# Performance work log

Hardware: AMD Instinct MI355X
Metric: run time of the kernel (lower is better)

The kernel has to match this reference:

```python
import jax, jax.numpy as jnp
import numpy as np

LRELU = 0.01  # torch nn.LeakyReLU default slope

def _lrelu(x):
    return jnp.where(x >= 0, x, LRELU * x)

def setup_inputs() -> dict:
    key = jax.random.key(0)
    ks = jax.random.split(key, 10)
    B, Cin, Cout, H, W, K, FD, LAT = 16, 256, 256, 64, 64, 3, 128, 128
    y = jax.random.normal(ks[0], (B, Cin, H, W), jnp.float32)
    finger = jax.random.randint(ks[1], (B, FD), 0, 2).astype(jnp.float32)
    ori_weight = jax.random.normal(ks[2], (Cout, Cin, K, K), jnp.float32) * 0.05
    w_mask = jax.random.normal(ks[3], (Cout, Cin, 1, 1), jnp.float32)
    f_weight = ori_weight[None]  # param initialized as 1*ori_weight, shape [1,Cout,Cin,K,K]
    style_w1 = jax.random.normal(ks[4], (LAT, FD), jnp.float32) / np.sqrt(FD)
    style_w2 = jax.random.normal(ks[5], (2 * Cin * K * K, LAT), jnp.float32) / np.sqrt(LAT)
    ori_bias = jax.random.normal(ks[6], (Cout,), jnp.float32) * 0.05
    b_mask = jax.random.normal(ks[7], (Cout,), jnp.float32)
    f_bias = ori_bias[None]  # [1,Cout]
    bias_w1 = jax.random.normal(ks[8], (Cout, FD), jnp.float32) / np.sqrt(FD)
    bias_w2 = jax.random.normal(ks[9], (Cout, Cout), jnp.float32) / np.sqrt(Cout)
    return dict(y=y, finger=finger, ori_weight=ori_weight, w_mask=w_mask,
                f_weight=f_weight, style_w1=style_w1, style_w2=style_w2,
                ori_bias=ori_bias, b_mask=b_mask, f_bias=f_bias,
                bias_w1=bias_w1, bias_w2=bias_w2)

def reference(y, finger, ori_weight, w_mask, f_weight, style_w1, style_w2,
              ori_bias, b_mask, f_bias, bias_w1, bias_w2):
    B = y.shape[0]
    Cout, Cin, K, _ = ori_weight.shape
    relu6 = lambda v: jnp.clip(v, 0.0, 6.0)
    # mask blending coefficients (w_mask broadcasts over the KxK taps, as in .repeat)
    f_w_weight = (6.0 - relu6(w_mask)) / 6.0          # [Cout,Cin,1,1]
    f_w_bias = (6.0 - relu6(b_mask)) / 6.0            # [Cout]
    mean_ori = ori_weight.mean()
    std_ori = jnp.std(ori_weight, ddof=1)             # torch .std() is unbiased
    # ApplyStyle: finger -> LAT -> 2*Cin*K*K scale/shift applied to f_weight
    h = _lrelu(finger @ style_w1.T)                   # [B,LAT]
    style = (h @ style_w2.T).reshape(B, 2, 1, Cin, K, K)
    s_weight = f_weight * (style[:, 0] + 1.0) + style[:, 1]  # [B,Cout,Cin,K,K]
    fw = f_w_weight[None]
    w1 = (1.0 - fw) * ori_weight[None] + fw * s_weight
    # per-sample whole-tensor re-standardization to ori stats
    mean = w1.mean(axis=(1, 2, 3, 4), keepdims=True)
    std = jnp.std(w1, axis=(1, 2, 3, 4), keepdims=True, ddof=1)
    w2 = (w1 - mean) / std * std_ori + mean_ori
    new_weight = (1.0 - fw) * ori_weight[None] + fw * w2      # [B,Cout,Cin,K,K]
    # per-sample bias
    s_bias = f_bias * _lrelu(_lrelu(finger @ bias_w1.T) @ bias_w2.T)  # [B,Cout]
    new_bias = (1.0 - f_w_bias) * ori_bias + f_w_bias * s_bias        # [B,Cout]
    pad = K // 2
    def conv_one(xi, wi, bi):
        o = jax.lax.conv_general_dilated(xi[None], wi, (1, 1),
                                         [(pad, pad), (pad, pad)],
                                         dimension_numbers=('NCHW', 'OIHW', 'NCHW'))
        return o[0] + bi[:, None, None]
    return jax.vmap(conv_one)(y, new_weight, new_bias)   # [B,Cout,H,W]
```

## Files before the change

### kernel.cpp

```cpp
#include <hip/hip_runtime.h>
#include <math.h>

#define LSLOPE 0.01f

__device__ __forceinline__ float lrelu(float x){ return x >= 0.f ? x : LSLOPE * x; }

typedef __attribute__((ext_vector_type(8))) short short8;
typedef __attribute__((ext_vector_type(4))) float f32x4;

__device__ __forceinline__ unsigned short f2bf(float f){
  union { float f; unsigned u; } v; v.f = f;
  unsigned r = v.u + 0x7FFFu + ((v.u >> 16) & 1u);
  return (unsigned short)(r >> 16);
}

__device__ __forceinline__ void gload_lds16(const unsigned short* g, unsigned short* l){
  __builtin_amdgcn_global_load_lds((const __attribute__((address_space(1))) unsigned int*)(g),
                                   (__attribute__((address_space(3))) unsigned int*)(l), 16, 0, 0);
}

constexpr int B    = 16;
constexpr int CIN  = 256;
constexpr int COUT = 256;
constexpr int HH   = 64;
constexpr int WW   = 64;
constexpr int FD   = 128;
constexpr int LAT  = 128;
constexpr int WPS  = CIN * 9;
constexpr int WTOT = COUT * WPS;
constexpr int HP   = 66;

constexpr int OFF_STAT  = 0;
constexpr int OFF_BMEAN = 16;
constexpr int OFF_BSTD  = 32;
constexpr int OFF_P     = 64;
constexpr int OFF_C     = OFF_P + 11 * 8 * WPS;
constexpr int OFF_STYLE = OFF_C + 11 * WPS;
constexpr int OFF_NBIAS = OFF_STYLE + B * 2 * WPS;
constexpr int OFF_NW    = OFF_NBIAS + B * COUT;
constexpr int OFF_YTR   = OFF_NW + (B * 9 * COUT * CIN) / 2;

__global__ __launch_bounds__(256) void k_coeff(const float* __restrict__ ow, const float* __restrict__ fwgt,
                                               const float* __restrict__ wmask, float* __restrict__ P){
  const int rb = blockIdx.x, ob = blockIdx.y;
  const int tid = threadIdx.x;
  const int rem = rb * 256 + tid;
  const int ic = rem / 9;
  float a_ow = 0.f, q_ow = 0.f, ab = 0.f, qb = 0.f;
  float a1 = 0.f, a2 = 0.f, d1 = 0.f, d2 = 0.f, d3 = 0.f, d4 = 0.f, d5 = 0.f;
  for (int oc = ob * 32; oc < ob * 32 + 32; ++oc){
    float w = ow[(size_t)oc * WPS + rem];
    float f = fwgt[(size_t)oc * WPS + rem];
    float m = wmask[oc * CIN + ic];
    float fw = (6.f - fminf(fmaxf(m, 0.f), 6.f)) * (1.f / 6.f);
    float base = w + fw * (f - w);
    float c1 = fw * f, c2 = fw;
    a_ow += w; q_ow += w * w;
    ab += base; qb += base * base;
    a1 += c1; a2 += c2;
    d1 += c1 * c1; d2 += c2 * c2; d3 += base * c1; d4 += base * c2; d5 += c1 * c2;
  }
  float* p = P + (size_t)ob * WPS + rem;
  p[(size_t)0  * 8 * WPS] = a_ow; p[(size_t)1  * 8 * WPS] = q_ow;
  p[(size_t)2  * 8 * WPS] = ab;   p[(size_t)3  * 8 * WPS] = qb;
  p[(size_t)4  * 8 * WPS] = a1;   p[(size_t)5  * 8 * WPS] = a2;
  p[(size_t)6  * 8 * WPS] = d1;   p[(size_t)7  * 8 * WPS] = d2;
  p[(size_t)8  * 8 * WPS] = d3;   p[(size_t)9  * 8 * WPS] = d4;
  p[(size_t)10 * 8 * WPS] = d5;
}

__global__ void k_coeff_r(const float* __restrict__ P, float* __restrict__ C){
  const int rem = blockIdx.x * 256 + threadIdx.x;
  #pragma unroll
  for (int a = 0; a < 11; ++a){
    float v = 0.f;
    for (int ob = 0; ob < 8; ++ob) v += P[((size_t)a * 8 + ob) * WPS + rem];
    C[(size_t)a * WPS + rem] = v;
  }
}

__global__ __launch_bounds__(256) void k_wstats(const float* __restrict__ C, const float* __restrict__ style,
                                                float* stat, float* bmean, float* bstd){
  __shared__ float rs[4][4];
  const int b = blockIdx.x, tid = threadIdx.x;
  const int lane = tid & 63, wid = tid >> 6;
  const float* st = style + (size_t)b * 2 * WPS;
  float s = 0.f, q = 0.f, so = 0.f, qo = 0.f;
  for (int k = 0; k < 9; ++k){
    int rem = k * 256 + tid;
    float aow = C[0 * WPS + rem], qow = C[1 * WPS + rem];
    float ab  = C[2 * WPS + rem], qb  = C[3 * WPS + rem];
    float a1  = C[4 * WPS + rem], a2  = C[5 * WPS + rem];
    float d1  = C[6 * WPS + rem], d2  = C[7 * WPS + rem];
    float d3  = C[8 * WPS + rem], d4  = C[9 * WPS + rem], d5 = C[10 * WPS + rem];
    float s0 = st[rem], s1 = st[WPS + rem];
    so += aow; qo += qow;
    s += ab + s0 * a1 + s1 * a2;
    q += qb + s0 * s0 * d1 + s1 * s1 * d2 + 2.f * (s0 * d3 + s1 * d4 + s0 * s1 * d5);
  }
  for (int o = 32; o > 0; o >>= 1){
    s += __shfl_down(s, o); q += __shfl_down(q, o);
    so += __shfl_down(so, o); qo += __shfl_down(qo, o);
  }
  if (lane == 0){ rs[0][wid] = s; rs[1][wid] = q; rs[2][wid] = so; rs[3][wid] = qo; }
  __syncthreads();
  if (tid == 0){
    const float N = (float)WTOT;
    float S = rs[0][0] + rs[0][1] + rs[0][2] + rs[0][3];
    float Q = rs[1][0] + rs[1][1] + rs[1][2] + rs[1][3];
    bmean[b] = S / N;
    bstd[b]  = sqrtf((Q - S * S / N) / (N - 1.f));
    if (b == 0){
      float SO = rs[2][0] + rs[2][1] + rs[2][2] + rs[2][3];
      float QO = rs[3][0] + rs[3][1] + rs[3][2] + rs[3][3];
      stat[0] = SO / N;
      stat[1] = sqrtf((QO - SO * SO / N) / (N - 1.f));
    }
  }
}

__global__ __launch_bounds__(256) void k_style2(const float* __restrict__ finger, const float* __restrict__ sw1,
                                                const float* __restrict__ sw2, float* __restrict__ style){
  __shared__ float hs[LAT];
  const int blk = blockIdx.x;
  const int b = blk / 18, j0 = (blk - b * 18) * 256;
  const int tid = threadIdx.x;
  if (tid < LAT){
    float a = 0.f;
    const float* fg = finger + b * FD;
    const float* w = sw1 + (size_t)tid * FD;
    for (int f = 0; f < FD; ++f) a += fg[f] * w[f];
    hs[tid] = lrelu(a);
  }
  __syncthreads();
  const int j = j0 + tid;
  float a = 0.f;
  const float* w2 = sw2 + (size_t)j * LAT;
  for (int l = 0; l < LAT; ++l) a += hs[l] * w2[l];
  style[(size_t)b * 2 * WPS + j] = a;
}

__global__ void k_bias(const float* __restrict__ finger, const float* __restrict__ bw1,
                       const float* __restrict__ bw2, const float* __restrict__ fbias,
                       const float* __restrict__ bmask, const float* __restrict__ obias,
                       float* __restrict__ nbias){
  __shared__ float hb[COUT];
  const int b = blockIdx.x, o = threadIdx.x;
  float acc = 0.f;
  for (int f = 0; f < FD; ++f) acc += finger[b * FD + f] * bw1[o * FD + f];
  hb[o] = lrelu(acc);
  __syncthreads();
  float t = 0.f;
  for (int c = 0; c < COUT; ++c) t += hb[c] * bw2[o * COUT + c];
  t = lrelu(t);
  float sb = fbias[o] * t;
  float fwb = (6.f - fminf(fmaxf(bmask[o], 0.f), 6.f)) * (1.f / 6.f);
  nbias[b * COUT + o] = (1.f - fwb) * obias[o] + fwb * sb;
}

__global__ __launch_bounds__(256) void k_new_weight2(const float* __restrict__ ow, const float* __restrict__ fwgt,
                                                     const float* __restrict__ wmask, const float* __restrict__ style,
                                                     const float* __restrict__ stat, const float* __restrict__ bmean,
                                                     const float* __restrict__ bstd, unsigned short* __restrict__ nw){
  __shared__ float ows[WPS];
  __shared__ float fws[WPS];
  const int b = blockIdx.x, oc = blockIdx.y;
  const int tid = threadIdx.x;
  const float mean_ori = stat[0], std_ori = stat[1];
  const float bm = bmean[b], bs = bstd[b];
  const float* owr = ow + (size_t)oc * WPS;
  const float* fwr = fwgt + (size_t)oc * WPS;
  for (int i = tid; i < WPS; i += 256){ ows[i] = owr[i]; fws[i] = fwr[i]; }
  const float fw = (6.f - fminf(fmaxf(wmask[oc * CIN + tid], 0.f), 6.f)) * (1.f / 6.f);
  const float* st = style + (size_t)b * 2 * WPS;
  __syncthreads();
  #pragma unroll
  for (int t = 0; t < 9; ++t){
    int rem = tid * 9 + t;
    float owv = ows[rem];
    float sw = fws[rem] * (st[rem] + 1.f) + st[WPS + rem];
    float w1 = owv + fw * (sw - owv);
    float w2 = (w1 - bm) / bs * std_ori + mean_ori;
    nw[((size_t)(b * 9 + t) * COUT + oc) * CIN + tid] = f2bf(owv + fw * (w2 - owv));
  }
}

constexpr int PADT = 264;
__global__ __launch_bounds__(256) void k_ytrp(const float* __restrict__ y, unsigned short* __restrict__ ytrp){
  __shared__ unsigned short t[64 * PADT];
  const int ghp = blockIdx.x;
  const int b = blockIdx.y;
  const int tid = threadIdx.x;
  unsigned short* dst = ytrp + ((size_t)b * HP + ghp) * HP * CIN;
  if (ghp == 0 || ghp == HP - 1){
    for (int c = tid; c < HP * CIN / 8; c += 256) ((uint4*)dst)[c] = (uint4){0, 0, 0, 0};
    return;
  }
  const int h = ghp - 1;
  const float* src = y + (size_t)b * CIN * HH * WW + h * WW;
  #pragma unroll
  for (int k = 0; k < 16; ++k){
    int idx = tid + k * 256;
    int ic = idx >> 4, w4 = (idx & 15) * 4;
    float4 v = *(const float4*)(src + (size_t)ic * HH * WW + w4);
    t[(w4 + 0) * PADT + ic] = f2bf(v.x);
    t[(w4 + 1) * PADT + ic] = f2bf(v.y);
    t[(w4 + 2) * PADT + ic] = f2bf(v.z);
    t[(w4 + 3) * PADT + ic] = f2bf(v.w);
  }
  __syncthreads();
  for (int c = tid; c < HP * CIN / 8; c += 256){
    int gwp = c >> 5, icg = (c & 31) * 8;
    uint4 v = (uint4){0, 0, 0, 0};
    if (gwp >= 1 && gwp <= 64) v = *(const uint4*)(&t[(gwp - 1) * PADT + icg]);
    ((uint4*)dst)[c] = v;
  }
}

__global__ __launch_bounds__(256, 2) void k_conv_mfma10(const unsigned short* __restrict__ ytrp,
                                                        const unsigned short* __restrict__ nw,
                                                        const float* __restrict__ nbias,
                                                        float* __restrict__ out){
  __shared__ __align__(16) unsigned short Wa[3 * 128 * 32];
  __shared__ __align__(16) unsigned short Yt[288 * 32];
  __shared__ float bsh[128];

  const int bid = blockIdx.x;
  const int xcd = bid & 7, idx = bid >> 3;
  const int grp = (idx & 3) * 8 + xcd;
  const int hwt = idx >> 2;
  const int b   = grp >> 1;
  const int oc0 = (grp & 1) * 128;
  const int tid = threadIdx.x;
  const int lane = tid & 63, wid = tid >> 6;
  const int wr = wid >> 1, wc = wid & 1;
  const int hw0 = hwt * 256;
  const int h0  = hwt * 4;

  if (tid < 128) bsh[tid] = nbias[b * COUT + oc0 + tid];

  f32x4 acc[4][8];
  #pragma unroll
  for (int i = 0; i < 4; ++i)
    #pragma unroll
    for (int j = 0; j < 8; ++j) acc[i][j] = (f32x4){0.f, 0.f, 0.f, 0.f};

  const unsigned short* nwb = nw + ((size_t)(b * 9) * COUT + oc0) * CIN;
  const unsigned short* ytb = ytrp + (size_t)b * HP * HP * CIN;

  int a_tap[6], a_go[6], a_lo[6];
  #pragma unroll
  for (int s = 0; s < 6; ++s){
    int I = wid + 4 * s;
    int tap = I >> 3, rowbase = (I & 7) * 16;
    int row = rowbase + (lane >> 2), p = lane & 3;
    int g = p ^ ((row >> 1) & 3);
    a_tap[s] = tap;
    a_go[s]  = row * CIN + g * 8;
    a_lo[s]  = (tap * 128 + rowbase) * 32;
  }
  int y_go[5], y_lo[5]; bool y_has[5];
  #pragma unroll
  for (int s = 0; s < 5; ++s){
    int I = wid + 4 * s;
    y_has[s] = (I < 18);
    int Ic = y_has[s] ? I : 0;
    int site = Ic * 16 + (lane >> 2);
    int srow = site / 72;
    int scol = site - srow * 72;
    int gwp  = scol > 65 ? 65 : scol;
    int p = lane & 3, g = p ^ ((site >> 1) & 3);
    y_go[s] = ((h0 + srow + 1) * HP + gwp) * CIN + g * 8;
    y_lo[s] = Ic * 16 * 32;
  }

  const int gq = lane >> 4;
  int a_rb[4];
  #pragma unroll
  for (int mi = 0; mi < 4; ++mi){
    int r = wr * 64 + mi * 16 + (lane & 15);
    a_rb[mi] = r * 64 + ((gq ^ ((r >> 1) & 3)) << 4);
  }
  int b_site[8];
  #pragma unroll
  for (int ni = 0; ni < 8; ++ni)
    b_site[ni] = (wc * 2 + (ni >> 2)) * 72 + (ni & 3) * 16 + (lane & 15);

  #define STAGE(IT)                                                                 \
    {                                                                               \
      const int dhb = (IT) >> 3;                                                    \
      const int ic0s = ((IT) & 7) * 32;                                             \
      const unsigned short* atap = nwb + (size_t)(dhb * 3) * COUT * CIN + ic0s;     \
      _Pragma("unroll")                                                             \
      for (int s = 0; s < 6; ++s)                                                   \
        gload_lds16(atap + (size_t)a_tap[s] * COUT * CIN + a_go[s], &Wa[0] + a_lo[s]); \
      const unsigned short* ybase = ytb + (ptrdiff_t)(dhb - 1) * HP * CIN + ic0s;   \
      _Pragma("unroll")                                                             \
      for (int s = 0; s < 5; ++s)                                                   \
        if (y_has[s]) gload_lds16(ybase + y_go[s], &Yt[0] + y_lo[s]);               \
    }

  #define COMPUTE()                                                                 \
    {                                                                               \
      const char* wap = (const char*)&Wa[0];                                        \
      const char* ytp = (const char*)&Yt[0];                                        \
      _Pragma("unroll")                                                             \
      for (int tap = 0; tap < 3; ++tap){                                            \
        short8 af[4];                                                               \
        _Pragma("unroll")                                                           \
        for (int mi = 0; mi < 4; ++mi)                                              \
          af[mi] = *(const short8*)(wap + tap * 8192 + a_rb[mi]);                   \
        _Pragma("unroll")                                                           \
        for (int ni = 0; ni < 8; ++ni){                                             \
          const int site = b_site[ni] + tap;                                        \
          const int boff = (site << 6) + ((gq ^ ((site >> 1) & 3)) << 4);           \
          const short8 bf = *(const short8*)(ytp + boff);                           \
          _Pragma("unroll")                                                         \
          for (int mi = 0; mi < 4; ++mi)                                            \
            acc[mi][ni] = __builtin_amdgcn_mfma_f32_16x16x32_bf16(af[mi], bf, acc[mi][ni], 0, 0, 0); \
        }                                                                           \
      }                                                                             \
    }

  #pragma unroll 1
  for (int it = 0; it < 24; ++it){
    __syncthreads();
    STAGE(it);
    __syncthreads();
    COMPUTE();
  }
  #undef STAGE
  #undef COMPUTE

  const int col_l = lane & 15, row_l = (lane >> 4) * 4;
  #pragma unroll
  for (int mi = 0; mi < 4; ++mi){
    #pragma unroll
    for (int r = 0; r < 4; ++r){
      const int ocl = wr * 64 + mi * 16 + row_l + r;
      const float bb = bsh[ocl];
      float* op = out + ((size_t)(b * COUT + oc0 + ocl)) * (HH * WW) + hw0 + wc * 128;
      #pragma unroll
      for (int ni = 0; ni < 8; ++ni)
        op[(ni >> 2) * 64 + (ni & 3) * 16 + col_l] = acc[mi][ni][r] + bb;
    }
  }
}

extern "C" void kernel_launch(void* const* d_in, const int* in_sizes, int n_in,
                              void* d_out, int out_size, void* d_ws, size_t ws_size,
                              hipStream_t stream){
  const float* y      = (const float*)d_in[0];
  const float* finger = (const float*)d_in[1];
  const float* ow     = (const float*)d_in[2];
  const float* wmask  = (const float*)d_in[3];
  const float* fwgt   = (const float*)d_in[4];
  const float* sw1    = (const float*)d_in[5];
  const float* sw2    = (const float*)d_in[6];
  const float* obias  = (const float*)d_in[7];
  const float* bmask  = (const float*)d_in[8];
  const float* fbias  = (const float*)d_in[9];
  const float* bw1    = (const float*)d_in[10];
  const float* bw2    = (const float*)d_in[11];
  float* out = (float*)d_out;
  float* ws  = (float*)d_ws;

  float* stat  = ws + OFF_STAT;
  float* bmean = ws + OFF_BMEAN;
  float* bstd  = ws + OFF_BSTD;
  float* P     = ws + OFF_P;
  float* C     = ws + OFF_C;
  float* style = ws + OFF_STYLE;
  float* nbias = ws + OFF_NBIAS;
  unsigned short* nw   = (unsigned short*)(ws + OFF_NW);
  unsigned short* ytrp = (unsigned short*)(ws + OFF_YTR);

  k_coeff<<<dim3(9, 8), 256, 0, stream>>>(ow, fwgt, wmask, P);
  k_coeff_r<<<9, 256, 0, stream>>>(P, C);
  k_style2<<<B * 18, 256, 0, stream>>>(finger, sw1, sw2, style);
  k_wstats<<<B, 256, 0, stream>>>(C, style, stat, bmean, bstd);
  k_bias<<<B, COUT, 0, stream>>>(finger, bw1, bw2, fbias, bmask, obias, nbias);
  k_new_weight2<<<dim3(B, COUT), 256, 0, stream>>>(ow, fwgt, wmask, style, stat, bmean, bstd, nw);
  k_ytrp<<<dim3(HP, B), 256, 0, stream>>>(y, ytrp);
  k_conv_mfma10<<<512, 256, 0, stream>>>(ytrp, nw, nbias, out);
}
```

Measured before the change: 150.7 us.

## Fuse style and bias kernels, batch weight gen, remap conv block order

Merges the style and bias MLP kernels into one launch to cut a kernel launch. The new-weight kernel now handles two batch samples per block and stages the style vectors in LDS, so the ori/f-weight loads are shared across samples. The conv kernel's block-to-(batch, oc, hw-tile) mapping is changed so each XCD holds fixed batches, which may improve L2 locality. The Y tile loads are also issued before the weight tile loads. The larger LDS footprint in the weight kernel may lower its occupancy.

```diff
diff --git a/kernel.cpp b/kernel.cpp
--- a/kernel.cpp
+++ b/kernel.cpp
@@ -119,69 +119,75 @@
   }
 }
 
-__global__ __launch_bounds__(256) void k_style2(const float* __restrict__ finger, const float* __restrict__ sw1,
-                                                const float* __restrict__ sw2, float* __restrict__ style){
-  __shared__ float hs[LAT];
+__global__ __launch_bounds__(256) void k_style_bias(const float* __restrict__ finger, const float* __restrict__ sw1,
+                                                    const float* __restrict__ sw2, float* __restrict__ style,
+                                                    const float* __restrict__ bw1, const float* __restrict__ bw2,
+                                                    const float* __restrict__ fbias, const float* __restrict__ bmask,
+                                                    const float* __restrict__ obias, float* __restrict__ nbias){
+  __shared__ float sh[COUT];
   const int blk = blockIdx.x;
-  const int b = blk / 18, j0 = (blk - b * 18) * 256;
-  const int tid = threadIdx.x;
-  if (tid < LAT){
+  const int tid = threadIdx.x;
+  if (blk < B * 18){
+    const int b = blk / 18, j0 = (blk - b * 18) * 256;
+    if (tid < LAT){
+      float a = 0.f;
+      const float* fg = finger + b * FD;
+      const float* w = sw1 + (size_t)tid * FD;
+      for (int f = 0; f < FD; ++f) a += fg[f] * w[f];
+      sh[tid] = lrelu(a);
+    }
+    __syncthreads();
+    const int j = j0 + tid;
     float a = 0.f;
-    const float* fg = finger + b * FD;
-    const float* w = sw1 + (size_t)tid * FD;
-    for (int f = 0; f < FD; ++f) a += fg[f] * w[f];
-    hs[tid] = lrelu(a);
-  }
-  __syncthreads();
-  const int j = j0 + tid;
-  float a = 0.f;
-  const float* w2 = sw2 + (size_t)j * LAT;
-  for (int l = 0; l < LAT; ++l) a += hs[l] * w2[l];
-  style[(size_t)b * 2 * WPS + j] = a;
-}
-
-__global__ void k_bias(const float* __restrict__ finger, const float* __restrict__ bw1,
-                       const float* __restrict__ bw2, const float* __restrict__ fbias,
-                       const float* __restrict__ bmask, const float* __restrict__ obias,
-                       float* __restrict__ nbias){
-  __shared__ float hb[COUT];
-  const int b = blockIdx.x, o = threadIdx.x;
-  float acc = 0.f;
-  for (int f = 0; f < FD; ++f) acc += finger[b * FD + f] * bw1[o * FD + f];
-  hb[o] = lrelu(acc);
-  __syncthreads();
-  float t = 0.f;
-  for (int c = 0; c < COUT; ++c) t += hb[c] * bw2[o * COUT + c];
-  t = lrelu(t);
-  float sb = fbias[o] * t;
-  float fwb = (6.f - fminf(fmaxf(bmask[o], 0.f), 6.f)) * (1.f / 6.f);
-  nbias[b * COUT + o] = (1.f - fwb) * obias[o] + fwb * sb;
-}
-
-__global__ __launch_bounds__(256) void k_new_weight2(const float* __restrict__ ow, const float* __restrict__ fwgt,
+    const float* w2 = sw2 + (size_t)j * LAT;
+    for (int l = 0; l < LAT; ++l) a += sh[l] * w2[l];
+    style[(size_t)b * 2 * WPS + j] = a;
+  } else {
+    const int b = blk - B * 18, o = tid;
+    float acc = 0.f;
+    for (int f = 0; f < FD; ++f) acc += finger[b * FD + f] * bw1[o * FD + f];
+    sh[o] = lrelu(acc);
+    __syncthreads();
+    float t = 0.f;
+    for (int c = 0; c < COUT; ++c) t += sh[c] * bw2[o * COUT + c];
+    t = lrelu(t);
+    float sb = fbias[o] * t;
+    float fwb = (6.f - fminf(fmaxf(bmask[o], 0.f), 6.f)) * (1.f / 6.f);
+    nbias[b * COUT + o] = (1.f - fwb) * obias[o] + fwb * sb;
+  }
+}
+
+__global__ __launch_bounds__(256) void k_new_weight4(const float* __restrict__ ow, const float* __restrict__ fwgt,
                                                      const float* __restrict__ wmask, const float* __restrict__ style,
                                                      const float* __restrict__ stat, const float* __restrict__ bmean,
                                                      const float* __restrict__ bstd, unsigned short* __restrict__ nw){
   __shared__ float ows[WPS];
   __shared__ float fws[WPS];
-  const int b = blockIdx.x, oc = blockIdx.y;
+  __shared__ float sts[2 * WPS];
+  const int bi = blockIdx.x, oc = blockIdx.y;
   const int tid = threadIdx.x;
   const float mean_ori = stat[0], std_ori = stat[1];
-  const float bm = bmean[b], bs = bstd[b];
   const float* owr = ow + (size_t)oc * WPS;
   const float* fwr = fwgt + (size_t)oc * WPS;
   for (int i = tid; i < WPS; i += 256){ ows[i] = owr[i]; fws[i] = fwr[i]; }
   const float fw = (6.f - fminf(fmaxf(wmask[oc * CIN + tid], 0.f), 6.f)) * (1.f / 6.f);
-  const float* st = style + (size_t)b * 2 * WPS;
-  __syncthreads();
-  #pragma unroll
-  for (int t = 0; t < 9; ++t){
-    int rem = tid * 9 + t;
-    float owv = ows[rem];
-    float sw = fws[rem] * (st[rem] + 1.f) + st[WPS + rem];
-    float w1 = owv + fw * (sw - owv);
-    float w2 = (w1 - bm) / bs * std_ori + mean_ori;
-    nw[((size_t)(b * 9 + t) * COUT + oc) * CIN + tid] = f2bf(owv + fw * (w2 - owv));
+  #pragma unroll
+  for (int bb = 0; bb < 2; ++bb){
+    const int b = bi * 2 + bb;
+    __syncthreads();
+    const float* st = style + (size_t)b * 2 * WPS;
+    for (int i = tid; i < 2 * WPS; i += 256) sts[i] = st[i];
+    __syncthreads();
+    const float bm = bmean[b], bs = bstd[b];
+    #pragma unroll
+    for (int t = 0; t < 9; ++t){
+      int rem = tid * 9 + t;
+      float owv = ows[rem];
+      float sw = fws[rem] * (sts[rem] + 1.f) + sts[WPS + rem];
+      float w1 = owv + fw * (sw - owv);
+      float w2 = (w1 - bm) / bs * std_ori + mean_ori;
+      nw[((size_t)(b * 9 + t) * COUT + oc) * CIN + tid] = f2bf(owv + fw * (w2 - owv));
+    }
   }
 }
 
@@ -217,7 +223,7 @@
   }
 }
 
-__global__ __launch_bounds__(256, 2) void k_conv_mfma10(const unsigned short* __restrict__ ytrp,
+__global__ __launch_bounds__(256, 2) void k_conv_mfma11(const unsigned short* __restrict__ ytrp,
                                                         const unsigned short* __restrict__ nw,
                                                         const float* __restrict__ nbias,
                                                         float* __restrict__ out){
@@ -226,11 +232,10 @@
   __shared__ float bsh[128];
 
   const int bid = blockIdx.x;
-  const int xcd = bid & 7, idx = bid >> 3;
-  const int grp = (idx & 3) * 8 + xcd;
-  const int hwt = idx >> 2;
-  const int b   = grp >> 1;
-  const int oc0 = (grp & 1) * 128;
+  const int xcd = bid & 7;
+  const int b   = ((bid >> 8) << 3) | xcd;
+  const int oc0 = ((bid >> 3) & 1) * 128;
+  const int hwt = (bid >> 4) & 15;
   const int tid = threadIdx.x;
   const int lane = tid & 63, wid = tid >> 6;
   const int wr = wid >> 1, wc = wid & 1;
@@ -290,14 +295,14 @@
     {                                                                               \
       const int dhb = (IT) >> 3;                                                    \
       const int ic0s = ((IT) & 7) * 32;                                             \
+      const unsigned short* ybase = ytb + (ptrdiff_t)(dhb - 1) * HP * CIN + ic0s;   \
+      _Pragma("unroll")                                                             \
+      for (int s = 0; s < 5; ++s)                                                   \
+        if (y_has[s]) gload_lds16(ybase + y_go[s], &Yt[0] + y_lo[s]);               \
       const unsigned short* atap = nwb + (size_t)(dhb * 3) * COUT * CIN + ic0s;     \
       _Pragma("unroll")                                                             \
       for (int s = 0; s < 6; ++s)                                                   \
         gload_lds16(atap + (size_t)a_tap[s] * COUT * CIN + a_go[s], &Wa[0] + a_lo[s]); \
-      const unsigned short* ybase = ytb + (ptrdiff_t)(dhb - 1) * HP * CIN + ic0s;   \
-      _Pragma("unroll")                                                             \
-      for (int s = 0; s < 5; ++s)                                                   \
-        if (y_has[s]) gload_lds16(ybase + y_go[s], &Yt[0] + y_lo[s]);               \
     }
 
   #define COMPUTE()                                                                 \
@@ -377,10 +382,9 @@
 
   k_coeff<<<dim3(9, 8), 256, 0, stream>>>(ow, fwgt, wmask, P);
   k_coeff_r<<<9, 256, 0, stream>>>(P, C);
-  k_style2<<<B * 18, 256, 0, stream>>>(finger, sw1, sw2, style);
+  k_style_bias<<<B * 18 + B, 256, 0, stream>>>(finger, sw1, sw2, style, bw1, bw2, fbias, bmask, obias, nbias);
   k_wstats<<<B, 256, 0, stream>>>(C, style, stat, bmean, bstd);
-  k_bias<<<B, COUT, 0, stream>>>(finger, bw1, bw2, fbias, bmask, obias, nbias);
-  k_new_weight2<<<dim3(B, COUT), 256, 0, stream>>>(ow, fwgt, wmask, style, stat, bmean, bstd, nw);
+  k_new_weight4<<<dim3(B / 2, COUT), 256, 0, stream>>>(ow, fwgt, wmask, style, stat, bmean, bstd, nw);
   k_ytrp<<<dim3(HP, B), 256, 0, stream>>>(y, ytrp);
-  k_conv_mfma10<<<512, 256, 0, stream>>>(ytrp, nw, nbias, out);
-}
+  k_conv_mfma11<<<512, 256, 0, stream>>>(ytrp, nw, nbias, out);
+}
```

After: 143.8 us. 1.05x faster.
